# Performance work log

Hardware: AMD Instinct MI355X
Metric: run time of the kernel (lower is better)

The kernel has to match this reference:

```python
import jax, jax.numpy as jnp
import numpy as np

D_MODEL = 2048
NUM_HEADS = 16
D_FF = 8192
BATCH = 4
SEQ = 2048


def setup_inputs() -> dict:
    key = jax.random.key(0)
    ks = jax.random.split(key, 16)
    s_attn = 1.0 / np.sqrt(D_MODEL)
    s_ff1 = 1.0 / np.sqrt(D_MODEL)
    s_ff2 = 1.0 / np.sqrt(D_FF)
    return {
        "x": jax.random.normal(ks[0], (BATCH, SEQ, D_MODEL), dtype=jnp.float32),
        "Wq": jax.random.normal(ks[1], (D_MODEL, D_MODEL), dtype=jnp.float32) * s_attn,
        "bq": jnp.zeros((D_MODEL,), dtype=jnp.float32),
        "Wk": jax.random.normal(ks[2], (D_MODEL, D_MODEL), dtype=jnp.float32) * s_attn,
        "bk": jnp.zeros((D_MODEL,), dtype=jnp.float32),
        "Wv": jax.random.normal(ks[3], (D_MODEL, D_MODEL), dtype=jnp.float32) * s_attn,
        "bv": jnp.zeros((D_MODEL,), dtype=jnp.float32),
        "Wo": jax.random.normal(ks[4], (D_MODEL, D_MODEL), dtype=jnp.float32) * s_attn,
        "bo": jnp.zeros((D_MODEL,), dtype=jnp.float32),
        "W1": jax.random.normal(ks[5], (D_MODEL, D_FF), dtype=jnp.float32) * s_ff1,
        "b1": jnp.zeros((D_FF,), dtype=jnp.float32),
        "W2": jax.random.normal(ks[6], (D_FF, D_MODEL), dtype=jnp.float32) * s_ff2,
        "b2": jnp.zeros((D_MODEL,), dtype=jnp.float32),
        "ln1_g": jnp.ones((D_MODEL,), dtype=jnp.float32),
        "ln1_b": jnp.zeros((D_MODEL,), dtype=jnp.float32),
        "ln2_g": jnp.ones((D_MODEL,), dtype=jnp.float32),
        "ln2_b": jnp.zeros((D_MODEL,), dtype=jnp.float32),
    }


def _layer_norm(x, g, b, eps=1e-5):
    mu = jnp.mean(x, axis=-1, keepdims=True)
    var = jnp.mean(jnp.square(x - mu), axis=-1, keepdims=True)
    return (x - mu) * jax.lax.rsqrt(var + eps) * g + b


def _attention(h, Wq, bq, Wk, bk, Wv, bv, Wo, bo):
    B, S, D = h.shape
    H = NUM_HEADS
    dk = D // H
    q = (h @ Wq + bq).reshape(B, S, H, dk).transpose(0, 2, 1, 3)  # bhsd
    k = (h @ Wk + bk).reshape(B, S, H, dk).transpose(0, 2, 1, 3)
    v = (h @ Wv + bv).reshape(B, S, H, dk).transpose(0, 2, 1, 3)
    logits = jnp.einsum("bhqd,bhkd->bhqk", q, k) / jnp.sqrt(jnp.float32(dk))
    causal = jnp.triu(jnp.ones((S, S), dtype=bool), k=1)  # True above diagonal
    logits = jnp.where(causal, -jnp.inf, logits)
    attn = jax.nn.softmax(logits, axis=-1)
    out = jnp.einsum("bhqk,bhkd->bhqd", attn, v)
    out = out.transpose(0, 2, 1, 3).reshape(B, S, D)
    return out @ Wo + bo


def reference(x, Wq, bq, Wk, bk, Wv, bv, Wo, bo, W1, b1, W2, b2,
              ln1_g, ln1_b, ln2_g, ln2_b):
    # Pre-LN attention block + residual
    h = _layer_norm(x, ln1_g, ln1_b)
    x = x + _attention(h, Wq, bq, Wk, bk, Wv, bv, Wo, bo)
    # Pre-LN FFN block + residual (GELU activation)
    h = _layer_norm(x, ln2_g, ln2_b)
    ff = jax.nn.gelu(h @ W1 + b1, approximate=False) @ W2 + b2
    return x + ff
```

## Files before the change

### kernel.cpp

```cpp
#include <hip/hip_runtime.h>
#include <hip/hip_bf16.h>

#define D_MODEL 2048
#define NUM_HEADS 16
#define D_FF 8192
#define BATCH 4
#define SEQ 2048
#define DK 128
#define MTOT (BATCH * SEQ)

typedef __attribute__((ext_vector_type(8))) short short8;
typedef __attribute__((ext_vector_type(4))) short short4v;
typedef __attribute__((ext_vector_type(4))) float f32x4;

#define MFMA16(a, b, c) __builtin_amdgcn_mfma_f32_16x16x32_bf16(a, b, c, 0, 0, 0)

#define GLOAD16(gp, lp)                                                        \
  __builtin_amdgcn_global_load_lds(                                            \
      (const __attribute__((address_space(1))) void*)(gp),                     \
      (__attribute__((address_space(3))) void*)(lp), 16, 0, 0)

static __device__ __forceinline__ unsigned short f2bf(float f) {
  return __builtin_bit_cast(unsigned short, __float2bfloat16(f));
}

__global__ __launch_bounds__(256) void transpose_cvt_kernel(
    const float* __restrict__ in, __hip_bfloat16* __restrict__ out, int K, int N) {
  __shared__ float tile[32][33];
  const int n0 = blockIdx.x * 32, k0 = blockIdx.y * 32;
  const int tx = threadIdx.x & 31, ty = threadIdx.x >> 5;
#pragma unroll
  for (int i = 0; i < 4; ++i)
    tile[ty + i * 8][tx] = in[(size_t)(k0 + ty + i * 8) * N + n0 + tx];
  __syncthreads();
#pragma unroll
  for (int i = 0; i < 4; ++i)
    out[(size_t)(n0 + ty + i * 8) * K + k0 + tx] = __float2bfloat16(tile[tx][ty + i * 8]);
}

__global__ __launch_bounds__(256) void layernorm_kernel(
    const float* __restrict__ x, const float* __restrict__ g,
    const float* __restrict__ bta, __hip_bfloat16* __restrict__ out) {
  const int row = blockIdx.x;
  const int tid = threadIdx.x;
  const float* xr = x + (size_t)row * D_MODEL;
  float4 v0 = *(const float4*)(xr + tid * 8);
  float4 v1 = *(const float4*)(xr + tid * 8 + 4);
  float s = v0.x + v0.y + v0.z + v0.w + v1.x + v1.y + v1.z + v1.w;
  float q = v0.x * v0.x + v0.y * v0.y + v0.z * v0.z + v0.w * v0.w +
            v1.x * v1.x + v1.y * v1.y + v1.z * v1.z + v1.w * v1.w;
#pragma unroll
  for (int off = 1; off < 64; off <<= 1) {
    s += __shfl_xor(s, off);
    q += __shfl_xor(q, off);
  }
  __shared__ float rs[4], rq[4];
  if ((tid & 63) == 0) {
    rs[tid >> 6] = s;
    rq[tid >> 6] = q;
  }
  __syncthreads();
  s = rs[0] + rs[1] + rs[2] + rs[3];
  q = rq[0] + rq[1] + rq[2] + rq[3];
  const float mu = s * (1.0f / D_MODEL);
  const float var = q * (1.0f / D_MODEL) - mu * mu;
  const float rstd = rsqrtf(var + 1e-5f);
  float4 g0 = *(const float4*)(g + tid * 8);
  float4 g1 = *(const float4*)(g + tid * 8 + 4);
  float4 b0 = *(const float4*)(bta + tid * 8);
  float4 b1 = *(const float4*)(bta + tid * 8 + 4);
  short8 o;
  o[0] = (short)f2bf((v0.x - mu) * rstd * g0.x + b0.x);
  o[1] = (short)f2bf((v0.y - mu) * rstd * g0.y + b0.y);
  o[2] = (short)f2bf((v0.z - mu) * rstd * g0.z + b0.z);
  o[3] = (short)f2bf((v0.w - mu) * rstd * g0.w + b0.w);
  o[4] = (short)f2bf((v1.x - mu) * rstd * g1.x + b1.x);
  o[5] = (short)f2bf((v1.y - mu) * rstd * g1.y + b1.y);
  o[6] = (short)f2bf((v1.z - mu) * rstd * g1.z + b1.z);
  o[7] = (short)f2bf((v1.w - mu) * rstd * g1.w + b1.w);
  *(short8*)(out + (size_t)row * D_MODEL + tid * 8) = o;
}

enum { EPI_BF16 = 0, EPI_VT = 1, EPI_RESID = 2, EPI_GELU = 3 };

template <int EPI>
__global__ __launch_bounds__(512, 2) void gemm_kernel(
    const __hip_bfloat16* __restrict__ A, const __hip_bfloat16* __restrict__ Bt,
    const float* __restrict__ bias, const float* __restrict__ resid,
    void* __restrict__ outv, int M, int N, int K) {
  __shared__ __align__(16) unsigned char lds[2][65536];
  const int tid = threadIdx.x;
  const int lane = tid & 63, w = tid >> 6;
  const int l15 = lane & 15, lg = lane >> 4;
  const int d = blockIdx.x;
  const int x = d & 7;
  const int i = d >> 3;
  const int cC = (i & 7) + 8 * (i >> 5);
  const int rC = x + 8 * ((i >> 3) & 3);
  const int m0 = rC * 256, n0 = cC * 256;
  const int wm = (w >> 2) * 128, wn = (w & 3) * 64;

  f32x4 acc[8][4] = {};

  const int row8 = lane >> 3;
  const int g8 = (lane & 7) ^ row8;

  auto STAGE = [&](int tt) {
    unsigned char* db = lds[tt & 1];
    const size_t ko = (size_t)tt * 64;
#pragma unroll
    for (int ii = 0; ii < 4; ++ii) {
      const int c = w * 4 + ii;
      const int row = c * 8 + row8;
      GLOAD16(A + (size_t)(m0 + row) * K + ko + g8 * 8, db + c * 1024);
    }
#pragma unroll
    for (int ii = 0; ii < 4; ++ii) {
      const int c = w * 4 + ii;
      const int row = c * 8 + row8;
      GLOAD16(Bt + (size_t)(n0 + row) * K + ko + g8 * 8, db + 32768 + c * 1024);
    }
  };
  auto COMPUTE = [&](int tt) {
    const unsigned char* db = lds[tt & 1];
#pragma unroll
    for (int ks = 0; ks < 2; ++ks) {
      const int cb = ks * 4 + lg;
      short8 af[8], bf[4];
#pragma unroll
      for (int f = 0; f < 8; ++f) {
        const int ra = wm + f * 16 + l15;
        af[f] = *(const short8*)(db + ra * 128 + ((cb ^ (ra & 7)) << 4));
      }
#pragma unroll
      for (int f = 0; f < 4; ++f) {
        const int rb = wn + f * 16 + l15;
        bf[f] = *(const short8*)(db + 32768 + rb * 128 + ((cb ^ (rb & 7)) << 4));
      }
      __builtin_amdgcn_s_setprio(1);
#pragma unroll
      for (int fi = 0; fi < 8; ++fi)
#pragma unroll
        for (int fj = 0; fj < 4; ++fj)
          acc[fi][fj] = MFMA16(af[fi], bf[fj], acc[fi][fj]);
      __builtin_amdgcn_s_setprio(0);
    }
  };

  const int nt = K >> 6;
  STAGE(0);
  STAGE(1);
  for (int t = 0; t < nt; ++t) {
    if (t < nt - 1)
      asm volatile("s_waitcnt vmcnt(8)" ::: "memory");
    else
      asm volatile("s_waitcnt vmcnt(0)" ::: "memory");
    __builtin_amdgcn_s_barrier();
    COMPUTE(t);
    asm volatile("" ::: "memory");
    __builtin_amdgcn_s_barrier();
    if (t + 2 < nt) STAGE(t + 2);
  }

#pragma unroll
  for (int fi = 0; fi < 8; ++fi) {
#pragma unroll
    for (int fj = 0; fj < 4; ++fj) {
      const int mb = m0 + wm + fi * 16 + lg * 4;
      const int n = n0 + wn + fj * 16 + l15;
      const float bv = bias ? bias[n] : 0.0f;
      if constexpr (EPI == EPI_VT) {
        const int bb = mb >> 11, ss = mb & (SEQ - 1);
        const int hh = n >> 7, dd = n & (DK - 1);
        short4v pk;
#pragma unroll
        for (int r = 0; r < 4; ++r) pk[r] = (short)f2bf(acc[fi][fj][r] + bv);
        __hip_bfloat16* o = (__hip_bfloat16*)outv;
        *(short4v*)(o + ((size_t)((bb * NUM_HEADS + hh) * DK + dd)) * SEQ + ss) = pk;
      } else {
#pragma unroll
        for (int r = 0; r < 4; ++r) {
          const int m = mb + r;
          const float v = acc[fi][fj][r] + bv;
          if constexpr (EPI == EPI_BF16) {
            ((__hip_bfloat16*)outv)[(size_t)m * N + n] = __float2bfloat16(v);
          } else if constexpr (EPI == EPI_GELU) {
            const float ge = 0.5f * v * (1.0f + erff(v * 0.70710678118654752f));
            ((__hip_bfloat16*)outv)[(size_t)m * N + n] = __float2bfloat16(ge);
          } else {
            ((float*)outv)[(size_t)m * N + n] = resid[(size_t)m * N + n] + v;
          }
        }
      }
    }
  }
}

__global__ __launch_bounds__(512, 4) void attn_kernel(
    const __hip_bfloat16* __restrict__ Qm, const __hip_bfloat16* __restrict__ Km,
    const __hip_bfloat16* __restrict__ Vt, __hip_bfloat16* __restrict__ Om) {
  __shared__ __align__(16) unsigned char Kl[2][16384];
  __shared__ __align__(16) unsigned char Vl[2][16384];
  __shared__ __align__(16) unsigned char Pl[16384];
  const int tid = threadIdx.x;
  const int lane = tid & 63, w = tid >> 6;
  const int l15 = lane & 15, lg = lane >> 4;
  const int bh = blockIdx.y, b = bh >> 4, h = bh & 15;
  const int q0 = ((int)gridDim.x - 1 - (int)blockIdx.x) * 128;
  const int qw = q0 + w * 16;
  const int row8 = lane >> 3;
  const int nt = (q0 >> 6) + 2;

  short8 qf[4];
  const __hip_bfloat16* qbase = Qm + (size_t)(b * SEQ + qw + l15) * D_MODEL + h * DK;
#pragma unroll
  for (int ks = 0; ks < 4; ++ks) qf[ks] = *(const short8*)(qbase + ks * 32 + lg * 8);

  float m_run[4], l_run[4];
  f32x4 acc_o[8];
#pragma unroll
  for (int r = 0; r < 4; ++r) { m_run[r] = -1e30f; l_run[r] = 0.0f; }
#pragma unroll
  for (int fd = 0; fd < 8; ++fd) acc_o[fd] = (f32x4){0.f, 0.f, 0.f, 0.f};

  auto STAGE = [&](int tt) {
    unsigned char* kb = Kl[tt & 1];
    unsigned char* vb = Vl[tt & 1];
    const int t0 = tt * 64;
#pragma unroll
    for (int i = 0; i < 2; ++i) {
      const int c = w * 2 + i;
      const int row = c * 4 + lg;
      const int gcb = l15 ^ (row & 7);
      GLOAD16(Km + (size_t)(b * SEQ + t0 + row) * D_MODEL + h * DK + gcb * 8,
              kb + c * 1024);
    }
#pragma unroll
    for (int i = 0; i < 2; ++i) {
      const int c = w * 2 + i;
      const int row = c * 8 + row8;
      const int gcb = (lane & 7) ^ (row & 7);
      GLOAD16(Vt + (size_t)(bh * DK + row) * SEQ + t0 + gcb * 8, vb + c * 1024);
    }
  };

  STAGE(0);
  for (int t = 0; t < nt; ++t) {
    const int t0 = t * 64;
    if (t + 1 < nt) {
      STAGE(t + 1);
      asm volatile("s_waitcnt vmcnt(4)" ::: "memory");
    } else {
      asm volatile("s_waitcnt vmcnt(0)" ::: "memory");
    }
    __builtin_amdgcn_s_barrier();
    asm volatile("" ::: "memory");
    if (t0 <= qw + 15) {
      const unsigned char* kb = Kl[t & 1];
      const unsigned char* vb = Vl[t & 1];
      f32x4 sacc[4];
#pragma unroll
      for (int fn = 0; fn < 4; ++fn) sacc[fn] = (f32x4){0.f, 0.f, 0.f, 0.f};
      __builtin_amdgcn_s_setprio(1);
#pragma unroll
      for (int ks = 0; ks < 4; ++ks) {
        const int cb = ks * 4 + lg;
#pragma unroll
        for (int fn = 0; fn < 4; ++fn) {
          const int rn = fn * 16 + l15;
          short8 kf = *(const short8*)(kb + rn * 256 + ((cb ^ (rn & 7)) << 4));
          sacc[fn] = MFMA16(qf[ks], kf, sacc[fn]);
        }
      }
      __builtin_amdgcn_s_setprio(0);
      const float scale = 0.088388347648318447f;
      float mt[4] = {-1e30f, -1e30f, -1e30f, -1e30f};
#pragma unroll
      for (int fn = 0; fn < 4; ++fn) {
        const int key = t0 + fn * 16 + l15;
#pragma unroll
        for (int r = 0; r < 4; ++r) {
          const int qg = qw + lg * 4 + r;
          float sv = sacc[fn][r] * scale;
          sv = (key <= qg) ? sv : -1e30f;
          sacc[fn][r] = sv;
          mt[r] = fmaxf(mt[r], sv);
        }
      }
#pragma unroll
      for (int r = 0; r < 4; ++r)
#pragma unroll
        for (int off = 1; off < 16; off <<= 1) mt[r] = fmaxf(mt[r], __shfl_xor(mt[r], off));
      int ok = 1;
#pragma unroll
      for (int r = 0; r < 4; ++r) ok = ok && (mt[r] <= m_run[r] + 8.0f);
      const bool defer = __all(ok);
      float alpha[4];
      if (!defer) {
#pragma unroll
        for (int r = 0; r < 4; ++r) {
          const float mnew = fmaxf(m_run[r], mt[r]);
          alpha[r] = __expf(m_run[r] - mnew);
          m_run[r] = mnew;
        }
      }
      float ls[4] = {0.f, 0.f, 0.f, 0.f};
#pragma unroll
      for (int fn = 0; fn < 4; ++fn)
#pragma unroll
        for (int r = 0; r < 4; ++r) {
          const float p = __expf(sacc[fn][r] - m_run[r]);
          sacc[fn][r] = p;
          ls[r] += p;
        }
#pragma unroll
      for (int r = 0; r < 4; ++r) {
#pragma unroll
        for (int off = 1; off < 16; off <<= 1) ls[r] += __shfl_xor(ls[r], off);
        l_run[r] = (defer ? l_run[r] : l_run[r] * alpha[r]) + ls[r];
      }
      if (!defer) {
#pragma unroll
        for (int fd = 0; fd < 8; ++fd)
#pragma unroll
          for (int r = 0; r < 4; ++r) acc_o[fd][r] *= alpha[r];
      }
      unsigned char* pw = Pl + w * 2048;
#pragma unroll
      for (int fn = 0; fn < 4; ++fn) {
        const int tt = fn * 16 + l15;
#pragma unroll
        for (int r = 0; r < 4; ++r) {
          const int qq = lg * 4 + r;
          *(unsigned short*)(pw + qq * 128 +
                             ((((tt >> 3) + qq + (qq >> 3)) & 7) << 4) +
                             (tt & 7) * 2) = f2bf(sacc[fn][r]);
        }
      }
#pragma unroll
      for (int ks = 0; ks < 2; ++ks) {
        const int tb = ks * 4 + lg;
        short8 pf = *(const short8*)(Pl + w * 2048 + l15 * 128 +
                                     (((tb + l15 + (l15 >> 3)) & 7) << 4));
        const int cb = ks * 4 + lg;
        __builtin_amdgcn_s_setprio(1);
#pragma unroll
        for (int fd = 0; fd < 8; ++fd) {
          const int rv = fd * 16 + l15;
          short8 vf = *(const short8*)(vb + rv * 128 + ((cb ^ (rv & 7)) << 4));
          acc_o[fd] = MFMA16(pf, vf, acc_o[fd]);
        }
        __builtin_amdgcn_s_setprio(0);
      }
    }
    asm volatile("" ::: "memory");
    __builtin_amdgcn_s_barrier();
    asm volatile("" ::: "memory");
  }
#pragma unroll
  for (int r = 0; r < 4; ++r) {
    const float inv = 1.0f / l_run[r];
    const int qg = qw + lg * 4 + r;
    __hip_bfloat16* ob = Om + (size_t)(b * SEQ + qg) * D_MODEL + h * DK + l15;
#pragma unroll
    for (int fd = 0; fd < 8; ++fd)
      ob[fd * 16] = __float2bfloat16(acc_o[fd][r] * inv);
  }
}

extern "C" void kernel_launch(void* const* d_in, const int* in_sizes, int n_in,
                              void* d_out, int out_size, void* d_ws, size_t ws_size,
                              hipStream_t stream) {
  (void)in_sizes; (void)n_in; (void)out_size;
  const size_t MB = 1024 * 1024;
  if (ws_size < 192 * MB) return;

  const float* x  = (const float*)d_in[0];
  const float* Wq = (const float*)d_in[1];
  const float* bq = (const float*)d_in[2];
  const float* Wk = (const float*)d_in[3];
  const float* bk = (const float*)d_in[4];
  const float* Wv = (const float*)d_in[5];
  const float* bv = (const float*)d_in[6];
  const float* Wo = (const float*)d_in[7];
  const float* bo = (const float*)d_in[8];
  const float* W1 = (const float*)d_in[9];
  const float* b1 = (const float*)d_in[10];
  const float* W2 = (const float*)d_in[11];
  const float* b2 = (const float*)d_in[12];
  const float* g1 = (const float*)d_in[13];
  const float* be1 = (const float*)d_in[14];
  const float* g2 = (const float*)d_in[15];
  const float* be2 = (const float*)d_in[16];

  char* ws = (char*)d_ws;
  __hip_bfloat16* Hb  = (__hip_bfloat16*)(ws + 0 * MB);
  __hip_bfloat16* Qb  = (__hip_bfloat16*)(ws + 32 * MB);
  __hip_bfloat16* Kb  = (__hip_bfloat16*)(ws + 64 * MB);
  __hip_bfloat16* Vtb = (__hip_bfloat16*)(ws + 96 * MB);
  __hip_bfloat16* AOb = (__hip_bfloat16*)(ws + 128 * MB);
  __hip_bfloat16* FF1 = (__hip_bfloat16*)(ws + 32 * MB);
  __hip_bfloat16* WqT = (__hip_bfloat16*)(ws + 160 * MB);
  __hip_bfloat16* WkT = (__hip_bfloat16*)(ws + 168 * MB);
  __hip_bfloat16* WvT = (__hip_bfloat16*)(ws + 176 * MB);
  __hip_bfloat16* WoT = (__hip_bfloat16*)(ws + 184 * MB);
  __hip_bfloat16* W1T = (__hip_bfloat16*)(ws + 160 * MB);
  __hip_bfloat16* W2T = (__hip_bfloat16*)(ws + 160 * MB);
  float* X2 = (float*)d_out;

  const dim3 tb(256);
  transpose_cvt_kernel<<<dim3(64, 64), tb, 0, stream>>>(Wq, WqT, 2048, 2048);
  transpose_cvt_kernel<<<dim3(64, 64), tb, 0, stream>>>(Wk, WkT, 2048, 2048);
  transpose_cvt_kernel<<<dim3(64, 64), tb, 0, stream>>>(Wv, WvT, 2048, 2048);
  transpose_cvt_kernel<<<dim3(64, 64), tb, 0, stream>>>(Wo, WoT, 2048, 2048);

  layernorm_kernel<<<MTOT, tb, 0, stream>>>(x, g1, be1, Hb);

  gemm_kernel<EPI_BF16><<<256, 512, 0, stream>>>(Hb, WqT, bq, nullptr, Qb, MTOT, 2048, 2048);
  gemm_kernel<EPI_BF16><<<256, 512, 0, stream>>>(Hb, WkT, bk, nullptr, Kb, MTOT, 2048, 2048);
  gemm_kernel<EPI_VT><<<256, 512, 0, stream>>>(Hb, WvT, bv, nullptr, Vtb, MTOT, 2048, 2048);

  attn_kernel<<<dim3(SEQ / 128, BATCH * NUM_HEADS), dim3(512), 0, stream>>>(Qb, Kb, Vtb, AOb);

  gemm_kernel<EPI_RESID><<<256, 512, 0, stream>>>(AOb, WoT, bo, x, X2, MTOT, 2048, 2048);

  layernorm_kernel<<<MTOT, tb, 0, stream>>>(X2, g2, be2, Hb);

  transpose_cvt_kernel<<<dim3(256, 64), tb, 0, stream>>>(W1, W1T, 2048, 8192);
  gemm_kernel<EPI_GELU><<<1024, 512, 0, stream>>>(Hb, W1T, b1, nullptr, FF1, MTOT, 8192, 2048);
  transpose_cvt_kernel<<<dim3(64, 256), tb, 0, stream>>>(W2, W2T, 8192, 2048);
  gemm_kernel<EPI_RESID><<<256, 512, 0, stream>>>(FF1, W2T, b2, X2, X2, MTOT, 2048, 8192);
}
```

Before: 1.251 ms.

## Interleave global-to-LDS staging with MFMA phases in GEMM main loop

Restructures the GEMM main loop into four MFMA phases per K-tile. The global_load_lds issues for the tile two steps ahead are spread between phases, and A fragments are loaded per phase. The goal is finer-grained overlap of memory traffic with MFMA work and less time stalled at one big barrier/waitcnt. It adds more barriers per iteration and a careful vmcnt accounting, including the stA(t+1, wa+12) issued late, which risks ordering or race bugs.

```diff
diff --git a/kernel.cpp b/kernel.cpp
--- a/kernel.cpp
+++ b/kernel.cpp
@@ -83,6 +83,31 @@
 
 enum { EPI_BF16 = 0, EPI_VT = 1, EPI_RESID = 2, EPI_GELU = 3 };
 
+#define AF_MFMA_PHASE(FI0)                                                     \
+  {                                                                            \
+    const int raA = wm + (FI0) * 16 + l15;                                     \
+    const int raB = wm + ((FI0) + 1) * 16 + l15;                               \
+    short8 aA0 = *(const short8*)(db + raA * 128 + ((lg ^ (raA & 7)) << 4));   \
+    short8 aB0 = *(const short8*)(db + raB * 128 + ((lg ^ (raB & 7)) << 4));   \
+    short8 aA1 =                                                               \
+        *(const short8*)(db + raA * 128 + (((4 + lg) ^ (raA & 7)) << 4));      \
+    short8 aB1 =                                                               \
+        *(const short8*)(db + raB * 128 + (((4 + lg) ^ (raB & 7)) << 4));      \
+    __builtin_amdgcn_s_barrier();                                              \
+    asm volatile("s_waitcnt lgkmcnt(0)" ::: "memory");                         \
+    __builtin_amdgcn_sched_barrier(0);                                         \
+    __builtin_amdgcn_s_setprio(1);                                             \
+    _Pragma("unroll") for (int fj = 0; fj < 4; ++fj)                           \
+        acc[FI0][fj] = MFMA16(aA0, bf0[fj], acc[FI0][fj]);                     \
+    _Pragma("unroll") for (int fj = 0; fj < 4; ++fj)                           \
+        acc[(FI0) + 1][fj] = MFMA16(aB0, bf0[fj], acc[(FI0) + 1][fj]);         \
+    _Pragma("unroll") for (int fj = 0; fj < 4; ++fj)                           \
+        acc[FI0][fj] = MFMA16(aA1, bf1[fj], acc[FI0][fj]);                     \
+    _Pragma("unroll") for (int fj = 0; fj < 4; ++fj)                           \
+        acc[(FI0) + 1][fj] = MFMA16(aB1, bf1[fj], acc[(FI0) + 1][fj]);         \
+    __builtin_amdgcn_s_setprio(0);                                             \
+  }
+
 template <int EPI>
 __global__ __launch_bounds__(512, 2) void gemm_kernel(
     const __hip_bfloat16* __restrict__ A, const __hip_bfloat16* __restrict__ Bt,
@@ -104,62 +129,55 @@
 
   const int row8 = lane >> 3;
   const int g8 = (lane & 7) ^ row8;
-
-  auto STAGE = [&](int tt) {
-    unsigned char* db = lds[tt & 1];
-    const size_t ko = (size_t)tt * 64;
-#pragma unroll
-    for (int ii = 0; ii < 4; ++ii) {
-      const int c = w * 4 + ii;
-      const int row = c * 8 + row8;
-      GLOAD16(A + (size_t)(m0 + row) * K + ko + g8 * 8, db + c * 1024);
-    }
-#pragma unroll
-    for (int ii = 0; ii < 4; ++ii) {
-      const int c = w * 4 + ii;
-      const int row = c * 8 + row8;
-      GLOAD16(Bt + (size_t)(n0 + row) * K + ko + g8 * 8, db + 32768 + c * 1024);
-    }
+  const int wa = (w & 3) + ((w >> 2) * 16);
+
+  auto stA = [&](int tt, int c) {
+    GLOAD16(A + (size_t)(m0 + c * 8 + row8) * K + (size_t)tt * 64 + g8 * 8,
+            lds[tt & 1] + c * 1024);
   };
-  auto COMPUTE = [&](int tt) {
-    const unsigned char* db = lds[tt & 1];
-#pragma unroll
-    for (int ks = 0; ks < 2; ++ks) {
-      const int cb = ks * 4 + lg;
-      short8 af[8], bf[4];
-#pragma unroll
-      for (int f = 0; f < 8; ++f) {
-        const int ra = wm + f * 16 + l15;
-        af[f] = *(const short8*)(db + ra * 128 + ((cb ^ (ra & 7)) << 4));
-      }
-#pragma unroll
-      for (int f = 0; f < 4; ++f) {
-        const int rb = wn + f * 16 + l15;
-        bf[f] = *(const short8*)(db + 32768 + rb * 128 + ((cb ^ (rb & 7)) << 4));
-      }
-      __builtin_amdgcn_s_setprio(1);
-#pragma unroll
-      for (int fi = 0; fi < 8; ++fi)
-#pragma unroll
-        for (int fj = 0; fj < 4; ++fj)
-          acc[fi][fj] = MFMA16(af[fi], bf[fj], acc[fi][fj]);
-      __builtin_amdgcn_s_setprio(0);
-    }
+  auto stB = [&](int tt, int c) {
+    GLOAD16(Bt + (size_t)(n0 + c * 8 + row8) * K + (size_t)tt * 64 + g8 * 8,
+            lds[tt & 1] + 32768 + c * 1024);
   };
 
   const int nt = K >> 6;
-  STAGE(0);
-  STAGE(1);
+
+  stB(0, w); stB(0, 8 + w); stA(0, wa);
+  stB(0, 16 + w); stB(0, 24 + w); stA(0, wa + 4);
+  stA(0, wa + 8); stA(0, wa + 12);
+  stB(1, w); stB(1, 8 + w); stA(1, wa);
+  stB(1, 16 + w); stB(1, 24 + w); stA(1, wa + 4);
+  stA(1, wa + 8);
+  asm volatile("s_waitcnt vmcnt(7)" ::: "memory");
+  __builtin_amdgcn_s_barrier();
+
   for (int t = 0; t < nt; ++t) {
-    if (t < nt - 1)
-      asm volatile("s_waitcnt vmcnt(8)" ::: "memory");
+    const unsigned char* db = lds[t & 1];
+    const bool s1 = (t + 1 < nt), s2 = (t + 2 < nt);
+    short8 bf0[4], bf1[4];
+    if (s1) stA(t + 1, wa + 12);
+#pragma unroll
+    for (int f = 0; f < 4; ++f) {
+      const int rb = wn + f * 16 + l15;
+      bf0[f] = *(const short8*)(db + 32768 + rb * 128 + ((lg ^ (rb & 7)) << 4));
+      bf1[f] =
+          *(const short8*)(db + 32768 + rb * 128 + (((4 + lg) ^ (rb & 7)) << 4));
+    }
+    AF_MFMA_PHASE(0)
+    __builtin_amdgcn_s_barrier();
+    if (s2) { stB(t + 2, w); stB(t + 2, 8 + w); stA(t + 2, wa); }
+    AF_MFMA_PHASE(2)
+    __builtin_amdgcn_s_barrier();
+    if (s2) { stB(t + 2, 16 + w); stB(t + 2, 24 + w); stA(t + 2, wa + 4); }
+    AF_MFMA_PHASE(4)
+    __builtin_amdgcn_s_barrier();
+    if (s2) stA(t + 2, wa + 8);
+    AF_MFMA_PHASE(6)
+    if (s2)
+      asm volatile("s_waitcnt vmcnt(7)" ::: "memory");
     else
       asm volatile("s_waitcnt vmcnt(0)" ::: "memory");
     __builtin_amdgcn_s_barrier();
-    COMPUTE(t);
-    asm volatile("" ::: "memory");
-    __builtin_amdgcn_s_barrier();
-    if (t + 2 < nt) STAGE(t + 2);
   }
 
 #pragma unroll
```

New measurement: 1.226 ms. 2.0% less time.
